# Kernel optimization log

Hardware: AMD Instinct MI355X
Metric: run time of the kernel (lower is better)

The kernel has to match this reference:

```python
import jax, jax.numpy as jnp
import numpy as np

DIM = 256; D_STATE = 16; D_CONV = 4; EXPAND = 2; NS = 64
D_INNER = EXPAND * DIM; DT_RANK = (DIM + 15) // 16
B_SZ = 2; H = 64; W = 64


def setup_inputs() -> dict:
    key = jax.random.key(0)
    ks = jax.random.split(key, 32)
    g = lambda i, shape, s=0.02: jax.random.normal(ks[i], shape, dtype=jnp.float32) * s
    inp = {}
    inp["x"] = jax.random.normal(ks[0], (B_SZ, DIM, H, W), dtype=jnp.float32)
    inp["ln_w"] = jnp.ones((DIM,), jnp.float32)
    inp["ln_b"] = jnp.zeros((DIM,), jnp.float32)
    inp["in_proj_w"] = g(1, (2 * D_INNER, DIM))
    for suf, base in (("", 2), ("_b", 10), ("_s", 18)):
        inp["conv_w" + suf] = g(base, (D_INNER, D_CONV), 0.1)
        inp["conv_b" + suf] = g(base + 1, (D_INNER,), 0.1)
        inp["x_proj_w" + suf] = g(base + 2, (DT_RANK + 2 * D_STATE, D_INNER))
        inp["dt_proj_w" + suf] = g(base + 3, (D_INNER, DT_RANK), 0.1)
        inp["dt_proj_b" + suf] = g(base + 4, (D_INNER,), 0.5)
        inp["D" + suf] = jnp.ones((D_INNER,), jnp.float32)
    A_log = jnp.tile(jnp.log(jnp.arange(1, D_STATE + 1, dtype=jnp.float32)), (D_INNER, 1))
    inp["A_log"] = A_log
    inp["A_log_b"] = A_log
    inp["A_log_s"] = A_log
    inp["out_proj_w"] = g(26, (DIM, D_INNER))
    return inp


def _silu(x):
    return x * jax.nn.sigmoid(x)


def _causal_conv(x, w, b):
    # x: (B, L, D); w: (D, K) depthwise causal conv along L
    K = w.shape[1]; L = x.shape[1]
    xp = jnp.pad(x, ((0, 0), (K - 1, 0), (0, 0)))
    y = b
    for k in range(K):
        y = y + xp[:, k:k + L, :] * w[:, k]
    return y


def _ssm_dir(x, z, conv_w, conv_b, x_proj_w, dt_proj_w, dt_proj_b, A_log, Dp):
    # one directional Mamba inner fn (no out_proj); x, z: (B, L, d_inner)
    Bsz, L, Din = x.shape
    xc = _silu(_causal_conv(x, conv_w, conv_b))
    x_dbl = xc @ x_proj_w.T  # (B, L, dt_rank + 2*d_state)
    dt_r = x_dbl[..., :DT_RANK]
    Bm = x_dbl[..., DT_RANK:DT_RANK + D_STATE]
    Cm = x_dbl[..., DT_RANK + D_STATE:]
    dt = jax.nn.softplus(dt_r @ dt_proj_w.T + dt_proj_b)  # (B, L, d_inner)
    A = -jnp.exp(A_log)  # (d_inner, d_state)

    def step(h, inp):
        dt_t, x_t, B_t, C_t = inp
        dA = jnp.exp(dt_t[..., None] * A)  # (B, d_inner, d_state)
        h = dA * h + (dt_t * x_t)[..., None] * B_t[:, None, :]
        return h, jnp.einsum('bds,bs->bd', h, C_t)

    h0 = jnp.zeros((Bsz, Din, D_STATE), x.dtype)
    _, ys = jax.lax.scan(step, h0, (dt.transpose(1, 0, 2), xc.transpose(1, 0, 2),
                                    Bm.transpose(1, 0, 2), Cm.transpose(1, 0, 2)))
    y = ys.transpose(1, 0, 2) + xc * Dp
    return y * _silu(z)


def reference(x, ln_w, ln_b, in_proj_w,
              conv_w, conv_b, x_proj_w, dt_proj_w, dt_proj_b, D,
              conv_w_b, conv_b_b, x_proj_w_b, dt_proj_w_b, dt_proj_b_b, D_b,
              conv_w_s, conv_b_s, x_proj_w_s, dt_proj_w_s, dt_proj_b_s, D_s,
              A_log, A_log_b, A_log_s, out_proj_w):
    Bsz, C, Hh, Ww = x.shape
    L = Hh * Ww
    xf = x.reshape(Bsz, C, L).transpose(0, 2, 1)  # (B, L, C)
    mu = xf.mean(-1, keepdims=True)
    var = ((xf - mu) ** 2).mean(-1, keepdims=True)
    xn = (xf - mu) / jnp.sqrt(var + 1e-5) * ln_w + ln_b
    xz = xn @ in_proj_w.T  # (B, L, 2*d_inner), shared across directions
    xin, z = xz[..., :D_INNER], xz[..., D_INNER:]
    # forward scan
    y_f = _ssm_dir(xin, z, conv_w, conv_b, x_proj_w, dt_proj_w, dt_proj_b, A_log, D)
    # backward scan (flip sequence, scan, flip back)
    y_b = _ssm_dir(xin[:, ::-1], z[:, ::-1], conv_w_b, conv_b_b, x_proj_w_b,
                   dt_proj_w_b, dt_proj_b_b, A_log_b, D_b)[:, ::-1]
    # slice-interleaved scan: 'b (s i) d -> b (i s) d' with s = NS slices
    def il(t):
        return t.reshape(Bsz, NS, L // NS, D_INNER).transpose(0, 2, 1, 3).reshape(Bsz, L, D_INNER)
    def dil(t):
        return t.reshape(Bsz, L // NS, NS, D_INNER).transpose(0, 2, 1, 3).reshape(Bsz, L, D_INNER)
    y_s = dil(_ssm_dir(il(xin), il(z), conv_w_s, conv_b_s, x_proj_w_s,
                       dt_proj_w_s, dt_proj_b_s, A_log_s, D_s))
    out = (y_f + y_b + y_s) @ out_proj_w.T  # (B, L, C)
    return x + out.transpose(0, 2, 1).reshape(Bsz, C, Hh, Ww)
```

## Files before the change

### kernel.cpp

```cpp
#include <hip/hip_runtime.h>
#include <hip/hip_bf16.h>
#include <cstdint>

#define B_SZ 2
#define DIM 256
#define L_SEQ 4096
#define D_INNER 512
#define DT_RANK 16
#define D_STATE 16
#define NCHUNK 128
#define CHUNK 32

static constexpr size_t SZ_BIG_SH = (size_t)B_SZ * L_SEQ * D_INNER;
static constexpr size_t F_DIR  = (size_t)B_SZ * NCHUNK * D_STATE * D_INNER;
static constexpr size_t SD_DIR = (size_t)B_SZ * NCHUNK * D_INNER;

typedef __attribute__((ext_vector_type(8))) short short8v;
typedef __attribute__((ext_vector_type(4))) short short4v;
typedef __attribute__((ext_vector_type(4))) float f32x4;

__device__ __forceinline__ float silu_f(float v) {
    return v / (1.0f + __expf(-v));
}
__device__ __forceinline__ float softplus_fast(float v) {
    return (v > 15.0f) ? v : __logf(1.0f + __expf(v));
}
__device__ __forceinline__ short f2bf(float f) {
    uint32_t u = __float_as_uint(f);
    u += 0x7fffu + ((u >> 16) & 1u);
    return (short)(u >> 16);
}
__device__ __forceinline__ float bf2f(short s) {
    return __uint_as_float(((uint32_t)(uint16_t)s) << 16);
}
__device__ __forceinline__ int dir_map(int p, int dm) {
    if (dm == 0) return p;
    if (dm == 1) return (L_SEQ - 1) - p;
    return ((p & 63) << 6) | (p >> 6);
}
__device__ __forceinline__ void pow_dA(float r1, float* dA) {
    const float r2 = r1 * r1, r4 = r2 * r2, r8 = r4 * r4;
    dA[0] = r1;         dA[1] = r2;         dA[2] = r2 * r1;    dA[3] = r4;
    dA[4] = r4 * r1;    dA[5] = r4 * r2;    dA[6] = r4 * dA[2]; dA[7] = r8;
    dA[8] = r8 * r1;    dA[9] = r8 * r2;    dA[10] = r8 * dA[2]; dA[11] = r8 * r4;
    dA[12] = r8 * dA[4]; dA[13] = r8 * dA[5]; dA[14] = r8 * dA[6]; dA[15] = r8 * r8;
}

__global__ __launch_bounds__(256) void k_cvt(
    const float* __restrict__ Wi, const float* __restrict__ Wo,
    const float* __restrict__ xp0, const float* __restrict__ xp1, const float* __restrict__ xp2,
    const float* __restrict__ dw0, const float* __restrict__ dw1, const float* __restrict__ dw2,
    short* __restrict__ Wib, short* __restrict__ Wob,
    short* __restrict__ xpwb, short* __restrict__ dtwb)
{
    const int idx = blockIdx.x * 256 + threadIdx.x;
    const float* src; short* dst; int off;
    if (idx < 65536)        { src = Wi; dst = Wib; off = idx; }
    else if (idx < 98304)   { src = Wo; dst = Wob; off = idx - 65536; }
    else if (idx < 116736)  {
        int k = idx - 98304; const int d = k / 6144; k -= d * 6144;
        src = d == 0 ? xp0 : (d == 1 ? xp1 : xp2);
        dst = xpwb + (size_t)d * 24576; off = k;
    } else {
        int k = idx - 116736; const int d = k / 2048; k -= d * 2048;
        src = d == 0 ? dw0 : (d == 1 ? dw1 : dw2);
        dst = dtwb + (size_t)d * 8192; off = k;
    }
    const float4 v = *(const float4*)(src + (size_t)off * 4);
    short4v p = {f2bf(v.x), f2bf(v.y), f2bf(v.z), f2bf(v.w)};
    *(short4v*)(dst + (size_t)off * 4) = p;
}

__global__ __launch_bounds__(256) void k_ln_t(
    const float* __restrict__ x, const float* __restrict__ lnw,
    const float* __restrict__ lnb, short* __restrict__ xnb)
{
    __shared__ float xt[64][257];
    __shared__ float red[2][4][64];
    __shared__ float muS[64], rsS[64];
    __shared__ float lnwS[DIM], lnbS[DIM];

    const int b  = blockIdx.x >> 6;
    const int l0 = (blockIdx.x & 63) << 6;
    const int t  = threadIdx.x;
    lnwS[t] = lnw[t]; lnbS[t] = lnb[t];

    const float* xb = x + (size_t)b * DIM * L_SEQ + l0;
#pragma unroll
    for (int it = 0; it < 16; ++it) {
        const int idx = it * 256 + t;
        const int c = idx >> 4, pos = (idx & 15) << 2;
        const float4 v = *(const float4*)(xb + (size_t)c * L_SEQ + pos);
        xt[pos + 0][c] = v.x; xt[pos + 1][c] = v.y;
        xt[pos + 2][c] = v.z; xt[pos + 3][c] = v.w;
    }
    __syncthreads();
    {
        const int l = t & 63, cq = t >> 6;
        float sum = 0.f, sq = 0.f;
        for (int c = cq * 64; c < cq * 64 + 64; ++c) {
            const float v = xt[l][c];
            sum += v; sq += v * v;
        }
        red[0][cq][l] = sum; red[1][cq][l] = sq;
    }
    __syncthreads();
    if (t < 64) {
        const float s  = red[0][0][t] + red[0][1][t] + red[0][2][t] + red[0][3][t];
        const float q2 = red[1][0][t] + red[1][1][t] + red[1][2][t] + red[1][3][t];
        const float mu  = s * (1.0f / DIM);
        const float var = q2 * (1.0f / DIM) - mu * mu;
        muS[t] = mu; rsS[t] = rsqrtf(var + 1e-5f);
    }
    __syncthreads();
#pragma unroll
    for (int it = 0; it < 32; ++it) {
        const int idx = it * 256 + t;
        const int l = idx >> 7, cp = (idx & 127) << 1;
        const float mu = muS[l], rs = rsS[l];
        short2 p;
        p.x = f2bf((xt[l][cp + 0] - mu) * rs * lnwS[cp + 0] + lnbS[cp + 0]);
        p.y = f2bf((xt[l][cp + 1] - mu) * rs * lnwS[cp + 1] + lnbS[cp + 1]);
        *(short2*)(xnb + (size_t)((b * L_SEQ) + l0 + l) * DIM + cp) = p;
    }
}

__global__ __launch_bounds__(256) void k_inproj_mfma(
    const short* __restrict__ xnb, const short* __restrict__ Wib,
    short* __restrict__ xinb, short* __restrict__ szb)
{
    const int mblk = blockIdx.x >> 2;
    const int q    = blockIdx.x & 3;
    const int t = threadIdx.x;
    const int w = t >> 6, l = t & 63;
    const int m0 = mblk * 64 + w * 16;
    const int n0 = q * 256;
    const int lrow = l & 15, lk = l >> 4;

    short8v a[8];
    {
        const short* ap = xnb + (size_t)(m0 + lrow) * DIM + lk * 8;
#pragma unroll
        for (int kk = 0; kk < 8; ++kk)
            a[kk] = *(const short8v*)(ap + kk * 32);
    }

#pragma unroll 4
    for (int nf = 0; nf < 16; ++nf) {
        const int n = n0 + nf * 16 + lrow;
        const short* bp = Wib + (size_t)n * DIM + lk * 8;
        f32x4 acc = {0.f, 0.f, 0.f, 0.f};
#pragma unroll
        for (int kk = 0; kk < 8; ++kk)
            acc = __builtin_amdgcn_mfma_f32_16x16x32_bf16(
                a[kk], *(const short8v*)(bp + kk * 32), acc, 0, 0, 0);
        const int col = n;
        const int r0  = m0 + lk * 4;
        if (n0 < D_INNER) {
#pragma unroll
            for (int j = 0; j < 4; ++j)
                xinb[(size_t)(r0 + j) * D_INNER + col] = f2bf(acc[j]);
        } else {
#pragma unroll
            for (int j = 0; j < 4; ++j)
                szb[(size_t)(r0 + j) * D_INNER + (col - D_INNER)] = f2bf(silu_f(acc[j]));
        }
    }
}

__global__ __launch_bounds__(256) void k_conv3(
    const short* __restrict__ xinb,
    const float* __restrict__ cw0, const float* __restrict__ cw1, const float* __restrict__ cw2,
    const float* __restrict__ cb0, const float* __restrict__ cb1, const float* __restrict__ cb2,
    short* __restrict__ xcbb, int dir_base, size_t xcb_str)
{
    const int rel = blockIdx.x >> 9;
    const int rem = blockIdx.x & 511;
    const int dir = dir_base + rel;
    const int b   = rem >> 8;
    const int p0  = (rem & 255) << 4;
    const int t   = threadIdx.x;

    const float* cw = dir == 0 ? cw0 : (dir == 1 ? cw1 : cw2);
    const float* cb = dir == 0 ? cb0 : (dir == 1 ? cb1 : cb2);
    short* xcb = xcbb + (size_t)rel * xcb_str;

    __shared__ short s[19][D_INNER];
    for (int i = 0; i < 19; ++i) {
        const int pk = p0 - 3 + i;
        short2 v = {0, 0};
        if (pk >= 0) {
            const int lo = dir_map(pk, dir);
            v = *(const short2*)(xinb + ((size_t)b * L_SEQ + lo) * D_INNER + t * 2);
        }
        *(short2*)&s[i][t * 2] = v;
    }
    __syncthreads();

#pragma unroll
    for (int half = 0; half < 2; ++half) {
        const int d = half * 256 + t;
        const float4 wv = *(const float4*)(cw + d * 4);
        const float bb = cb[d];
        float x0 = bf2f(s[0][d]), x1 = bf2f(s[1][d]), x2 = bf2f(s[2][d]);
#pragma unroll
        for (int i = 0; i < 16; ++i) {
            const float x3 = bf2f(s[i + 3][d]);
            const float a = bb + wv.x * x0 + wv.y * x1 + wv.z * x2 + wv.w * x3;
            xcb[((size_t)b * L_SEQ + p0 + i) * D_INNER + d] = f2bf(silu_f(a));
            x0 = x1; x1 = x2; x2 = x3;
        }
    }
}

__global__ __launch_bounds__(256) void k_proj3_mfma(
    const short* __restrict__ xcbb, const short* __restrict__ xpwb,
    const short* __restrict__ dtwb,
    const float* __restrict__ dtb0, const float* __restrict__ dtb1, const float* __restrict__ dtb2,
    short* __restrict__ dtYb, float* __restrict__ bcbuf,
    int dir_base, size_t xcb_str, size_t bc_str)
{
    const int rel = blockIdx.x >> 9;
    const int rem = blockIdx.x & 511;
    const int dir = dir_base + rel;
    const int m0  = rem * 16;
    const int t = threadIdx.x;
    const int w = t >> 6, l = t & 63;
    const int lrow = l & 15, lk = l >> 4;

    const short* xcb = xcbb + (size_t)rel * xcb_str;
    const short* xpw = xpwb + (size_t)dir * (48 * 512);
    const short* dtw = dtwb + (size_t)dir * (512 * 16);
    const float* dtb = dir == 0 ? dtb0 : (dir == 1 ? dtb1 : dtb2);
    short* dt = dtYb + (size_t)dir * SZ_BIG_SH;
    float* bc = bcbuf + (size_t)rel * bc_str;

    __shared__ float red[4][3][16][17];
    __shared__ short xdblb[16][16];
    __shared__ float dtbS[512];

    dtbS[t] = dtb[t]; dtbS[t + 256] = dtb[t + 256];

    short8v a[4];
    {
        const short* ap = xcb + (size_t)(m0 + lrow) * D_INNER + w * 128 + lk * 8;
#pragma unroll
        for (int kk = 0; kk < 4; ++kk)
            a[kk] = *(const short8v*)(ap + kk * 32);
    }

#pragma unroll
    for (int nf = 0; nf < 3; ++nf) {
        f32x4 acc = {0.f, 0.f, 0.f, 0.f};
        const short* bp = xpw + (size_t)(nf * 16 + lrow) * D_INNER + w * 128 + lk * 8;
#pragma unroll
        for (int kk = 0; kk < 4; ++kk)
            acc = __builtin_amdgcn_mfma_f32_16x16x32_bf16(
                a[kk], *(const short8v*)(bp + kk * 32), acc, 0, 0, 0);
#pragma unroll
        for (int j = 0; j < 4; ++j)
            red[w][nf][lk * 4 + j][lrow] = acc[j];
    }
    __syncthreads();

#pragma unroll
    for (int i = 0; i < 3; ++i) {
        const int nf = i;
        const int row = (t >> 4) & 15, col = t & 15;
        const float v = red[0][nf][row][col] + red[1][nf][row][col]
                      + red[2][nf][row][col] + red[3][nf][row][col];
        if (nf == 0) xdblb[row][col] = f2bf(v);
        else         bc[(size_t)(m0 + row) * 32 + (nf - 1) * 16 + col] = v;
    }
    __syncthreads();

    short8v adt = {0, 0, 0, 0, 0, 0, 0, 0};
    if (lk < 2) adt = *(const short8v*)&xdblb[lrow][lk * 8];

#pragma unroll
    for (int nbw = 0; nbw < 8; ++nbw) {
        const int nb = w * 8 + nbw;
        short8v bdt = {0, 0, 0, 0, 0, 0, 0, 0};
        if (lk < 2) bdt = *(const short8v*)(dtw + (size_t)(nb * 16 + lrow) * 16 + lk * 8);
        f32x4 acc = {0.f, 0.f, 0.f, 0.f};
        acc = __builtin_amdgcn_mfma_f32_16x16x32_bf16(adt, bdt, acc, 0, 0, 0);
        const int d = nb * 16 + lrow;
        const float bias = dtbS[d];
#pragma unroll
        for (int j = 0; j < 4; ++j)
            dt[(size_t)(m0 + lk * 4 + j) * D_INNER + d] = f2bf(softplus_fast(acc[j] + bias));
    }
}

__device__ __forceinline__ bool fast_vote(const float* Al_d, int t, int* flagS) {
    bool ok = true;
    const float a0 = __expf(Al_d[0]);
#pragma unroll
    for (int s = 1; s < 16; ++s) {
        const float v = __expf(Al_d[s]);
        const float e = (float)(s + 1) * a0;
        ok = ok && (fabsf(v - e) <= 1e-3f * e);
    }
    if (t == 0) *flagS = 1;
    __syncthreads();
    if (!ok) *flagS = 0;
    __syncthreads();
    return *flagS != 0;
}

template<bool FAST>
__device__ __forceinline__ void scan1_body(
    const short* dtp, const short* xcp, const float* bcp,
    short (*dts)[256], short (*xcs)[256], float (*bcs)[16],
    const float* Al_d, int t, short* F_o, float* SD_o)
{
    float As20, As2[16];
    if (FAST) {
        As20 = -__expf(Al_d[0]) * 1.44269504f;
    } else {
#pragma unroll
        for (int s = 0; s < 16; ++s) As2[s] = -__expf(Al_d[s]) * 1.44269504f;
        As20 = As2[0];
    }
    float h[16];
#pragma unroll
    for (int s = 0; s < 16; ++s) h[s] = 0.f;
    float sumdt = 0.f;

    for (int tile = 0; tile < CHUNK / 16; ++tile) {
        const int p0 = tile * 16;
#pragma unroll
        for (int rep = 0; rep < 2; ++rep) {
            const int idx = rep * 256 + t;
            const int jr = idx >> 5, c8 = (idx & 31) << 3;
            *(short8v*)&dts[jr][c8] = *(const short8v*)(dtp + (size_t)(p0 + jr) * D_INNER + c8);
            *(short8v*)&xcs[jr][c8] = *(const short8v*)(xcp + (size_t)(p0 + jr) * D_INNER + c8);
        }
        if (t < 64) {
            const int jr = t >> 2, c4 = (t & 3) << 2;
            *(float4*)&bcs[jr][c4] = *(const float4*)(bcp + (size_t)(p0 + jr) * 32 + c4);
        }
        __syncthreads();

#pragma unroll
        for (int j = 0; j < 16; ++j) {
            const float dtv = bf2f(dts[j][t]);
            const float xv  = bf2f(xcs[j][t]);
            sumdt += dtv;
            const float dtx = dtv * xv;
            float Bv[16];
#pragma unroll
            for (int s4 = 0; s4 < 4; ++s4) {
                const float4 bb = *(const float4*)&bcs[j][s4 * 4];
                Bv[s4 * 4 + 0] = bb.x; Bv[s4 * 4 + 1] = bb.y;
                Bv[s4 * 4 + 2] = bb.z; Bv[s4 * 4 + 3] = bb.w;
            }
            if (FAST) {
                float dA[16];
                pow_dA(exp2f(dtv * As20), dA);
#pragma unroll
                for (int s = 0; s < 16; ++s)
                    h[s] = fmaf(dA[s], h[s], dtx * Bv[s]);
            } else {
#pragma unroll
                for (int s = 0; s < 16; ++s)
                    h[s] = fmaf(exp2f(dtv * As2[s]), h[s], dtx * Bv[s]);
            }
        }
        __syncthreads();
    }
#pragma unroll
    for (int s = 0; s < 16; ++s)
        F_o[(size_t)s * D_INNER] = f2bf(h[s]);
    *SD_o = sumdt;
}

template<bool FAST>
__device__ __forceinline__ void scan2_body(
    short* dtp, const short* xcp, const float* bcp,
    short (*dts)[256], short (*xcs)[256], float (*bcs)[32],
    const float* Al_d, int t, float Dv, const short* Hin_o)
{
    float As20, As2[16];
    if (FAST) {
        As20 = -__expf(Al_d[0]) * 1.44269504f;
    } else {
#pragma unroll
        for (int s = 0; s < 16; ++s) As2[s] = -__expf(Al_d[s]) * 1.44269504f;
        As20 = As2[0];
    }
    float h[16];
#pragma unroll
    for (int s = 0; s < 16; ++s)
        h[s] = bf2f(Hin_o[(size_t)s * D_INNER]);

    for (int tile = 0; tile < CHUNK / 16; ++tile) {
        const int p0 = tile * 16;
#pragma unroll
        for (int rep = 0; rep < 2; ++rep) {
            const int idx = rep * 256 + t;
            const int jr = idx >> 5, c8 = (idx & 31) << 3;
            *(short8v*)&dts[jr][c8] = __builtin_nontemporal_load(
                (const short8v*)(dtp + (size_t)(p0 + jr) * D_INNER + c8));
            *(short8v*)&xcs[jr][c8] = __builtin_nontemporal_load(
                (const short8v*)(xcp + (size_t)(p0 + jr) * D_INNER + c8));
        }
        if (t < 128) {
            const int jr = t >> 3, c4 = (t & 7) << 2;
            *(float4*)&bcs[jr][c4] = *(const float4*)(bcp + (size_t)(p0 + jr) * 32 + c4);
        }
        __syncthreads();

#pragma unroll
        for (int j = 0; j < 16; ++j) {
            const float dtv = bf2f(dts[j][t]);
            const float xv  = bf2f(xcs[j][t]);
            const float dtx = dtv * xv;
            float Bv[16], Cv[16];
#pragma unroll
            for (int s4 = 0; s4 < 4; ++s4) {
                const float4 bb = *(const float4*)&bcs[j][s4 * 4];
                const float4 cc = *(const float4*)&bcs[j][16 + s4 * 4];
                Bv[s4 * 4 + 0] = bb.x; Bv[s4 * 4 + 1] = bb.y;
                Bv[s4 * 4 + 2] = bb.z; Bv[s4 * 4 + 3] = bb.w;
                Cv[s4 * 4 + 0] = cc.x; Cv[s4 * 4 + 1] = cc.y;
                Cv[s4 * 4 + 2] = cc.z; Cv[s4 * 4 + 3] = cc.w;
            }
            float y = xv * Dv;
            if (FAST) {
                float dA[16];
                pow_dA(exp2f(dtv * As20), dA);
#pragma unroll
                for (int s = 0; s < 16; ++s) {
                    h[s] = fmaf(dA[s], h[s], dtx * Bv[s]);
                    y = fmaf(h[s], Cv[s], y);
                }
            } else {
#pragma unroll
                for (int s = 0; s < 16; ++s) {
                    h[s] = fmaf(exp2f(dtv * As2[s]), h[s], dtx * Bv[s]);
                    y = fmaf(h[s], Cv[s], y);
                }
            }
            __builtin_nontemporal_store(f2bf(y), dtp + (size_t)(p0 + j) * D_INNER + t);
        }
        __syncthreads();
    }
}

__global__ __launch_bounds__(256, 4) void k_scan1(
    const short* __restrict__ dtYb, const short* __restrict__ xcbb,
    const float* __restrict__ bcb,
    const float* __restrict__ Al0, const float* __restrict__ Al1, const float* __restrict__ Al2,
    short* __restrict__ Fg, float* __restrict__ SDg,
    int dir_base, size_t xcb_str, size_t bc_str)
{
    const int rel = blockIdx.x >> 9;
    const int rem = blockIdx.x & 511;
    const int dir = dir_base + rel;
    const int b     = rem >> 8;
    const int chunk = (rem >> 1) & 127;
    const int half  = rem & 1;
    const int t = threadIdx.x;
    const int d = half * 256 + t;

    const short* dtg = dtYb + (size_t)dir * SZ_BIG_SH;
    const short* xcg = xcbb + (size_t)rel * xcb_str;
    const float* bcg = bcb + (size_t)rel * bc_str;
    const float* Al = dir == 0 ? Al0 : (dir == 1 ? Al1 : Al2);
    short* F  = Fg  + (size_t)rel * F_DIR;
    float* SD = SDg + (size_t)rel * SD_DIR;

    __shared__ short dts[16][256];
    __shared__ short xcs[16][256];
    __shared__ float bcs[16][16];
    __shared__ int flagS;

    const size_t rowbase = (size_t)b * L_SEQ + chunk * CHUNK;
    const short* dtp = dtg + rowbase * D_INNER + half * 256;
    const short* xcp = xcg + rowbase * D_INNER + half * 256;
    const float* bcp = bcg + rowbase * 32;
    const float* Al_d = Al + d * D_STATE;
    const size_t fo  = ((size_t)b * NCHUNK + chunk) * (D_STATE * D_INNER) + d;
    const size_t sdo = ((size_t)b * NCHUNK + chunk) * D_INNER + d;

    const bool fast = fast_vote(Al_d, t, &flagS);
    if (fast) scan1_body<true >(dtp, xcp, bcp, dts, xcs, bcs, Al_d, t, F + fo, SD + sdo);
    else      scan1_body<false>(dtp, xcp, bcp, dts, xcs, bcs, Al_d, t, F + fo, SD + sdo);
}

__global__ __launch_bounds__(256) void k_comb(
    short* __restrict__ Fg, const float* __restrict__ SDg,
    const float* __restrict__ Al0, const float* __restrict__ Al1, const float* __restrict__ Al2,
    int dir_base)
{
    const int rel = blockIdx.x >> 6;
    const int dir = dir_base + rel;
    const int gid = (blockIdx.x & 63) * 256 + threadIdx.x;
    const int b   = gid >> 13;
    const int rem = gid & 8191;
    const int s   = rem >> 9;
    const int d   = rem & 511;

    const float* Al = dir == 0 ? Al0 : (dir == 1 ? Al1 : Al2);
    const float As2 = -__expf(Al[d * D_STATE + s]) * 1.44269504f;

    short* F        = Fg  + (size_t)rel * F_DIR;
    const float* SD = SDg + (size_t)rel * SD_DIR;

    float h = 0.f;
    for (int c = 0; c < NCHUNK; ++c) {
        const size_t base = (size_t)(b * NCHUNK + c);
        const size_t i  = (base << 13) + rem;
        const float sd  = SD[(base << 9) + d];
        const float P   = exp2f(As2 * sd);
        const float fv  = bf2f(F[i]);
        F[i] = f2bf(h);
        h = fmaf(P, h, fv);
    }
}

__global__ __launch_bounds__(256, 4) void k_scan2(
    short* dtYb,
    const short* __restrict__ xcbb, const float* __restrict__ bcb,
    const float* __restrict__ Al0, const float* __restrict__ Al1, const float* __restrict__ Al2,
    const float* __restrict__ Dp0, const float* __restrict__ Dp1, const float* __restrict__ Dp2,
    const short* __restrict__ Hing,
    int dir_base, size_t xcb_str, size_t bc_str)
{
    const int rel = blockIdx.x >> 9;
    const int rem = blockIdx.x & 511;
    const int dir = dir_base + rel;
    const int b     = rem >> 8;
    const int chunk = (rem >> 1) & 127;
    const int half  = rem & 1;
    const int t = threadIdx.x;
    const int d = half * 256 + t;

    short* dtg      = dtYb + (size_t)dir * SZ_BIG_SH;
    const short* xcg = xcbb + (size_t)rel * xcb_str;
    const float* bcg = bcb + (size_t)rel * bc_str;
    const float* Al  = dir == 0 ? Al0 : (dir == 1 ? Al1 : Al2);
    const float* Dpp = dir == 0 ? Dp0 : (dir == 1 ? Dp1 : Dp2);
    const short* Hin = Hing + (size_t)rel * F_DIR;

    __shared__ short dts[16][256];
    __shared__ short xcs[16][256];
    __shared__ float bcs[16][32];
    __shared__ int flagS;

    const size_t rowbase = (size_t)b * L_SEQ + chunk * CHUNK;
    short* dtp       = dtg + rowbase * D_INNER + half * 256;
    const short* xcp = xcg + rowbase * D_INNER + half * 256;
    const float* bcp = bcg + rowbase * 32;
    const float* Al_d = Al + d * D_STATE;
    const float Dv = Dpp[d];
    const size_t fo = ((size_t)b * NCHUNK + chunk) * (D_STATE * D_INNER) + d;

    const bool fast = fast_vote(Al_d, t, &flagS);
    if (fast) scan2_body<true >(dtp, xcp, bcp, dts, xcs, bcs, Al_d, t, Dv, Hin + fo);
    else      scan2_body<false>(dtp, xcp, bcp, dts, xcs, bcs, Al_d, t, Dv, Hin + fo);
}

__global__ __launch_bounds__(256) void k_out3_mfma(
    const short* __restrict__ yall, const short* __restrict__ szb,
    const short* __restrict__ Wob, const float* __restrict__ x,
    float* __restrict__ out)
{
    __shared__ short ytb[32][512];
    const int tile = blockIdx.x;
    const int b  = tile >> 7;
    const int l0 = (tile & 127) << 5;
    const int t  = threadIdx.x;

    const short* y0 = yall;
    const short* y1 = yall + SZ_BIG_SH;
    const short* y2 = yall + 2 * SZ_BIG_SH;
    const size_t rb = (size_t)b * L_SEQ;

#pragma unroll
    for (int it = 0; it < 8; ++it) {
        const int idx = it * 256 + t;
        const int r  = idx >> 6;
        const int c8 = idx & 63;
        const int lrow = l0 + r;
        const int p1 = (L_SEQ - 1) - lrow;
        const int p2 = ((lrow & 63) << 6) | (lrow >> 6);
        const short8v s0 = *(const short8v*)(y0 + (rb + lrow) * D_INNER + c8 * 8);
        const short8v s1 = *(const short8v*)(y1 + (rb + p1)   * D_INNER + c8 * 8);
        const short8v s2 = *(const short8v*)(y2 + (rb + p2)   * D_INNER + c8 * 8);
        const short8v sv = *(const short8v*)(szb + (rb + lrow) * D_INNER + c8 * 8);
        short8v pk;
#pragma unroll
        for (int i = 0; i < 8; ++i)
            pk[i] = f2bf((bf2f(s0[i]) + bf2f(s1[i]) + bf2f(s2[i])) * bf2f(sv[i]));
        *(short8v*)&ytb[r][(c8 ^ (r & 7)) * 8] = pk;
    }
    __syncthreads();

    const int w = t >> 6, l = t & 63;
    const int lrow = l & 15, lk = l >> 4;
    const int nf = w & 1;
    const int j0 = (w >> 1) * 128;
    const int brow = nf * 16 + lrow;

    f32x4 acc[8];
#pragma unroll
    for (int jf = 0; jf < 8; ++jf) acc[jf] = {0.f, 0.f, 0.f, 0.f};

#pragma unroll 4
    for (int kk = 0; kk < 16; ++kk) {
        const int c8 = kk * 4 + lk;
        const short8v bfrag = *(const short8v*)&ytb[brow][(c8 ^ (brow & 7)) * 8];
#pragma unroll
        for (int jf = 0; jf < 8; ++jf) {
            const short8v afrag = *(const short8v*)(
                Wob + (size_t)(j0 + jf * 16 + lrow) * D_INNER + kk * 32 + lk * 8);
            acc[jf] = __builtin_amdgcn_mfma_f32_16x16x32_bf16(afrag, bfrag, acc[jf], 0, 0, 0);
        }
    }

    const int lcol = l0 + nf * 16 + lrow;
#pragma unroll
    for (int jf = 0; jf < 8; ++jf) {
        const int jr0 = j0 + jf * 16 + lk * 4;
#pragma unroll
        for (int j = 0; j < 4; ++j) {
            const size_t o = ((size_t)b * DIM + jr0 + j) * L_SEQ + lcol;
            out[o] = x[o] + acc[jf][j];
        }
    }
}

extern "C" void kernel_launch(void* const* d_in, const int* in_sizes, int n_in,
                              void* d_out, int out_size, void* d_ws, size_t ws_size,
                              hipStream_t stream)
{
    const float* x       = (const float*)d_in[0];
    const float* ln_w    = (const float*)d_in[1];
    const float* ln_b    = (const float*)d_in[2];
    const float* in_proj = (const float*)d_in[3];
    const float* conv_w[3] = {(const float*)d_in[4],  (const float*)d_in[10], (const float*)d_in[16]};
    const float* conv_b[3] = {(const float*)d_in[5],  (const float*)d_in[11], (const float*)d_in[17]};
    const float* xpw[3]    = {(const float*)d_in[6],  (const float*)d_in[12], (const float*)d_in[18]};
    const float* dtw[3]    = {(const float*)d_in[7],  (const float*)d_in[13], (const float*)d_in[19]};
    const float* dtb[3]    = {(const float*)d_in[8],  (const float*)d_in[14], (const float*)d_in[20]};
    const float* Dp[3]     = {(const float*)d_in[9],  (const float*)d_in[15], (const float*)d_in[21]};
    const float* A_log[3]  = {(const float*)d_in[22], (const float*)d_in[23], (const float*)d_in[24]};
    const float* out_proj  = (const float*)d_in[25];
    float* out = (float*)d_out;
    (void)in_sizes; (void)n_in; (void)out_size;

    const size_t NROW   = (size_t)B_SZ * L_SEQ;
    const size_t SZ_XNB = NROW * DIM / 2;
    const size_t SZ_WIB = 262144 / 2;
    const size_t SZ_WOB = 131072 / 2;
    const size_t SZ_XPW = 3 * 24576 / 2;
    const size_t SZ_DTW = 3 * 8192 / 2;
    const size_t SZ_BH  = NROW * D_INNER / 2;
    const size_t SZ_BC  = NROW * 32;
    const size_t SZ_F   = F_DIR / 2;

    const size_t need_merged =
        SZ_XNB + SZ_WIB + SZ_WOB + SZ_XPW + SZ_DTW +
        2 * SZ_BH + 3 * SZ_BH + 3 * SZ_BH + 3 * SZ_BC +
        3 * (SZ_F + SD_DIR);
    const bool merged = ws_size >= need_merged * sizeof(float);
    const int ndir = merged ? 3 : 1;
    const size_t xcb_str = merged ? (SZ_BH * 2) : 0;
    const size_t bc_str  = merged ? SZ_BC : 0;

    float* ws   = (float*)d_ws;
    float* p    = ws;
    short* xnb  = (short*)p;  p += SZ_XNB;
    short* Wib  = (short*)p;  p += SZ_WIB;
    short* Wob  = (short*)p;  p += SZ_WOB;
    short* xpwb = (short*)p;  p += SZ_XPW;
    short* dtwb = (short*)p;  p += SZ_DTW;
    short* xinb = (short*)p;  p += SZ_BH;
    short* szb  = (short*)p;  p += SZ_BH;
    short* dtYb = (short*)p;  p += 3 * SZ_BH;
    short* xcbb = (short*)p;  p += (size_t)ndir * SZ_BH;
    float* bc   = p;          p += (size_t)ndir * SZ_BC;
    short* Fg   = (short*)p;  p += (size_t)ndir * SZ_F;
    float* SDg  = p;          p += (size_t)ndir * SD_DIR;

    k_cvt<<<dim3(480), dim3(256), 0, stream>>>(
        in_proj, out_proj, xpw[0], xpw[1], xpw[2], dtw[0], dtw[1], dtw[2],
        Wib, Wob, xpwb, dtwb);
    k_ln_t<<<dim3(B_SZ * 64), dim3(256), 0, stream>>>(x, ln_w, ln_b, xnb);
    k_inproj_mfma<<<dim3(512), dim3(256), 0, stream>>>(xnb, Wib, xinb, szb);

    for (int d0 = 0; d0 < 3; d0 += ndir) {
        k_conv3<<<dim3(512 * ndir), dim3(256), 0, stream>>>(
            xinb, conv_w[0], conv_w[1], conv_w[2],
            conv_b[0], conv_b[1], conv_b[2], xcbb, d0, xcb_str);
        k_proj3_mfma<<<dim3(512 * ndir), dim3(256), 0, stream>>>(
            xcbb, xpwb, dtwb, dtb[0], dtb[1], dtb[2],
            dtYb, bc, d0, xcb_str, bc_str);
        k_scan1<<<dim3(512 * ndir), dim3(256), 0, stream>>>(
            dtYb, xcbb, bc, A_log[0], A_log[1], A_log[2], Fg, SDg,
            d0, xcb_str, bc_str);
        k_comb<<<dim3(64 * ndir), dim3(256), 0, stream>>>(
            Fg, SDg, A_log[0], A_log[1], A_log[2], d0);
        k_scan2<<<dim3(512 * ndir), dim3(256), 0, stream>>>(
            dtYb, xcbb, bc, A_log[0], A_log[1], A_log[2],
            Dp[0], Dp[1], Dp[2], Fg, d0, xcb_str, bc_str);
    }

    k_out3_mfma<<<dim3(256), dim3(256), 0, stream>>>(
        dtYb, szb, Wob, x, out);
}
```

Measured before the change: 232.8 us.

## Fuse x/dt projection with chunk-local scan pass and halve chunk length

Merges the projection kernel with the first chunked-scan pass. The dt, xc and B/C tiles for a 16-row chunk stay in shared memory (dt with an XOR swizzle) and feed the local scan directly, so the scan no longer re-reads them from global memory and one launch per direction goes away. The chunk size drops from 32 to 16, which doubles the chunk count. That doubles the work of the serial chunk-combine pass and the size of the F/SD buffers, and each fused block now has every thread scan two channels, adding shared memory and register pressure.

Result: slower. 261.6 us (+12.4%).

```diff
diff --git a/kernel.cpp b/kernel.cpp
--- a/kernel.cpp
+++ b/kernel.cpp
@@ -8,8 +8,8 @@
 #define D_INNER 512
 #define DT_RANK 16
 #define D_STATE 16
-#define NCHUNK 128
-#define CHUNK 32
+#define NCHUNK 256
+#define CHUNK 16
 
 static constexpr size_t SZ_BIG_SH = (size_t)B_SZ * L_SEQ * D_INNER;
 static constexpr size_t F_DIR  = (size_t)B_SZ * NCHUNK * D_STATE * D_INNER;
@@ -213,17 +213,70 @@
     }
 }
 
-__global__ __launch_bounds__(256) void k_proj3_mfma(
+template<bool FAST>
+__device__ __forceinline__ void chunk_scan_local(
+    const short (*dtS)[512], const short (*xcS)[512], const float (*bcsS)[32],
+    const float* Al_d, int d, short* F_o, float* SD_o)
+{
+    float As20, As2[16];
+    if (FAST) {
+        As20 = -__expf(Al_d[0]) * 1.44269504f;
+    } else {
+#pragma unroll
+        for (int s = 0; s < 16; ++s) As2[s] = -__expf(Al_d[s]) * 1.44269504f;
+        As20 = As2[0];
+    }
+    float h[16];
+#pragma unroll
+    for (int s = 0; s < 16; ++s) h[s] = 0.f;
+    float sumdt = 0.f;
+
+#pragma unroll
+    for (int j = 0; j < 16; ++j) {
+        const float dtv = bf2f(dtS[j][d ^ (j << 3)]);
+        const float xv  = bf2f(xcS[j][d]);
+        sumdt += dtv;
+        const float dtx = dtv * xv;
+        float Bv[16];
+#pragma unroll
+        for (int s4 = 0; s4 < 4; ++s4) {
+            const float4 bb = *(const float4*)&bcsS[j][s4 * 4];
+            Bv[s4 * 4 + 0] = bb.x; Bv[s4 * 4 + 1] = bb.y;
+            Bv[s4 * 4 + 2] = bb.z; Bv[s4 * 4 + 3] = bb.w;
+        }
+        if (FAST) {
+            float dA[16];
+            pow_dA(exp2f(dtv * As20), dA);
+#pragma unroll
+            for (int s = 0; s < 16; ++s)
+                h[s] = fmaf(dA[s], h[s], dtx * Bv[s]);
+        } else {
+#pragma unroll
+            for (int s = 0; s < 16; ++s)
+                h[s] = fmaf(exp2f(dtv * As2[s]), h[s], dtx * Bv[s]);
+        }
+    }
+#pragma unroll
+    for (int s = 0; s < 16; ++s)
+        F_o[(size_t)s * D_INNER] = f2bf(h[s]);
+    *SD_o = sumdt;
+}
+
+__global__ __launch_bounds__(256) void k_proj_scan1(
     const short* __restrict__ xcbb, const short* __restrict__ xpwb,
     const short* __restrict__ dtwb,
     const float* __restrict__ dtb0, const float* __restrict__ dtb1, const float* __restrict__ dtb2,
+    const float* __restrict__ Al0, const float* __restrict__ Al1, const float* __restrict__ Al2,
     short* __restrict__ dtYb, float* __restrict__ bcbuf,
+    short* __restrict__ Fg, float* __restrict__ SDg,
     int dir_base, size_t xcb_str, size_t bc_str)
 {
     const int rel = blockIdx.x >> 9;
     const int rem = blockIdx.x & 511;
     const int dir = dir_base + rel;
     const int m0  = rem * 16;
+    const int b     = rem >> 8;
+    const int chunk = rem & 255;
     const int t = threadIdx.x;
     const int w = t >> 6, l = t & 63;
     const int lrow = l & 15, lk = l >> 4;
@@ -232,14 +285,29 @@
     const short* xpw = xpwb + (size_t)dir * (48 * 512);
     const short* dtw = dtwb + (size_t)dir * (512 * 16);
     const float* dtb = dir == 0 ? dtb0 : (dir == 1 ? dtb1 : dtb2);
+    const float* Al  = dir == 0 ? Al0 : (dir == 1 ? Al1 : Al2);
     short* dt = dtYb + (size_t)dir * SZ_BIG_SH;
     float* bc = bcbuf + (size_t)rel * bc_str;
-
+    short* F  = Fg  + (size_t)rel * F_DIR;
+    float* SD = SDg + (size_t)rel * SD_DIR;
+
+    __shared__ short xcS[16][512];
+    __shared__ short dtS[16][512];
     __shared__ float red[4][3][16][17];
     __shared__ short xdblb[16][16];
+    __shared__ float bcsS[16][32];
     __shared__ float dtbS[512];
-
+    __shared__ int flagS;
+
+#pragma unroll
+    for (int it = 0; it < 4; ++it) {
+        const int idx = it * 256 + t;
+        const int jr = idx >> 6, c8 = idx & 63;
+        *(short8v*)&xcS[jr][c8 * 8] =
+            *(const short8v*)(xcb + (size_t)(m0 + jr) * D_INNER + c8 * 8);
+    }
     dtbS[t] = dtb[t]; dtbS[t + 256] = dtb[t + 256];
+    __syncthreads();
 
     short8v a[4];
     {
@@ -269,8 +337,12 @@
         const int row = (t >> 4) & 15, col = t & 15;
         const float v = red[0][nf][row][col] + red[1][nf][row][col]
                       + red[2][nf][row][col] + red[3][nf][row][col];
-        if (nf == 0) xdblb[row][col] = f2bf(v);
-        else         bc[(size_t)(m0 + row) * 32 + (nf - 1) * 16 + col] = v;
+        if (nf == 0) {
+            xdblb[row][col] = f2bf(v);
+        } else {
+            bc[(size_t)(m0 + row) * 32 + (nf - 1) * 16 + col] = v;
+            bcsS[row][(nf - 1) * 16 + col] = v;
+        }
     }
     __syncthreads();
 
@@ -284,209 +356,50 @@
         if (lk < 2) bdt = *(const short8v*)(dtw + (size_t)(nb * 16 + lrow) * 16 + lk * 8);
         f32x4 acc = {0.f, 0.f, 0.f, 0.f};
         acc = __builtin_amdgcn_mfma_f32_16x16x32_bf16(adt, bdt, acc, 0, 0, 0);
-        const int d = nb * 16 + lrow;
-        const float bias = dtbS[d];
-#pragma unroll
-        for (int j = 0; j < 4; ++j)
-            dt[(size_t)(m0 + lk * 4 + j) * D_INNER + d] = f2bf(softplus_fast(acc[j] + bias));
-    }
-}
-
-__device__ __forceinline__ bool fast_vote(const float* Al_d, int t, int* flagS) {
+        const int dd = nb * 16 + lrow;
+        const float bias = dtbS[dd];
+#pragma unroll
+        for (int j = 0; j < 4; ++j) {
+            const int row = lk * 4 + j;
+            const short v = f2bf(softplus_fast(acc[j] + bias));
+            dt[(size_t)(m0 + row) * D_INNER + dd] = v;
+            dtS[row][dd ^ (row << 3)] = v;
+        }
+    }
+    __syncthreads();
+
     bool ok = true;
-    const float a0 = __expf(Al_d[0]);
-#pragma unroll
-    for (int s = 1; s < 16; ++s) {
-        const float v = __expf(Al_d[s]);
-        const float e = (float)(s + 1) * a0;
-        ok = ok && (fabsf(v - e) <= 1e-3f * e);
-    }
-    if (t == 0) *flagS = 1;
-    __syncthreads();
-    if (!ok) *flagS = 0;
-    __syncthreads();
-    return *flagS != 0;
-}
-
-template<bool FAST>
-__device__ __forceinline__ void scan1_body(
-    const short* dtp, const short* xcp, const float* bcp,
-    short (*dts)[256], short (*xcs)[256], float (*bcs)[16],
-    const float* Al_d, int t, short* F_o, float* SD_o)
-{
-    float As20, As2[16];
-    if (FAST) {
-        As20 = -__expf(Al_d[0]) * 1.44269504f;
+    {
+        const float* a0p = Al + t * D_STATE;
+        const float* a1p = Al + (t + 256) * D_STATE;
+        const float e00 = __expf(a0p[0]), e10 = __expf(a1p[0]);
+#pragma unroll
+        for (int s = 1; s < 16; ++s) {
+            const float v0 = __expf(a0p[s]), ex0 = (float)(s + 1) * e00;
+            const float v1 = __expf(a1p[s]), ex1 = (float)(s + 1) * e10;
+            ok = ok && (fabsf(v0 - ex0) <= 1e-3f * ex0)
+                    && (fabsf(v1 - ex1) <= 1e-3f * ex1);
+        }
+    }
+    if (t == 0) flagS = 1;
+    __syncthreads();
+    if (!ok) flagS = 0;
+    __syncthreads();
+    const bool fast = flagS != 0;
+
+    const size_t fbase  = ((size_t)b * NCHUNK + chunk) * (D_STATE * D_INNER);
+    const size_t sdbase = ((size_t)b * NCHUNK + chunk) * D_INNER;
+    if (fast) {
+        chunk_scan_local<true >(dtS, xcS, bcsS, Al + t * D_STATE, t,
+                                F + fbase + t, SD + sdbase + t);
+        chunk_scan_local<true >(dtS, xcS, bcsS, Al + (t + 256) * D_STATE, t + 256,
+                                F + fbase + t + 256, SD + sdbase + t + 256);
     } else {
-#pragma unroll
-        for (int s = 0; s < 16; ++s) As2[s] = -__expf(Al_d[s]) * 1.44269504f;
-        As20 = As2[0];
-    }
-    float h[16];
-#pragma unroll
-    for (int s = 0; s < 16; ++s) h[s] = 0.f;
-    float sumdt = 0.f;
-
-    for (int tile = 0; tile < CHUNK / 16; ++tile) {
-        const int p0 = tile * 16;
-#pragma unroll
-        for (int rep = 0; rep < 2; ++rep) {
-            const int idx = rep * 256 + t;
-            const int jr = idx >> 5, c8 = (idx & 31) << 3;
-            *(short8v*)&dts[jr][c8] = *(const short8v*)(dtp + (size_t)(p0 + jr) * D_INNER + c8);
-            *(short8v*)&xcs[jr][c8] = *(const short8v*)(xcp + (size_t)(p0 + jr) * D_INNER + c8);
-        }
-        if (t < 64) {
-            const int jr = t >> 2, c4 = (t & 3) << 2;
-            *(float4*)&bcs[jr][c4] = *(const float4*)(bcp + (size_t)(p0 + jr) * 32 + c4);
-        }
-        __syncthreads();
-
-#pragma unroll
-        for (int j = 0; j < 16; ++j) {
-            const float dtv = bf2f(dts[j][t]);
-            const float xv  = bf2f(xcs[j][t]);
-            sumdt += dtv;
-            const float dtx = dtv * xv;
-            float Bv[16];
-#pragma unroll
-            for (int s4 = 0; s4 < 4; ++s4) {
-                const float4 bb = *(const float4*)&bcs[j][s4 * 4];
-                Bv[s4 * 4 + 0] = bb.x; Bv[s4 * 4 + 1] = bb.y;
-                Bv[s4 * 4 + 2] = bb.z; Bv[s4 * 4 + 3] = bb.w;
-            }
-            if (FAST) {
-                float dA[16];
-                pow_dA(exp2f(dtv * As20), dA);
-#pragma unroll
-                for (int s = 0; s < 16; ++s)
-                    h[s] = fmaf(dA[s], h[s], dtx * Bv[s]);
-            } else {
-#pragma unroll
-                for (int s = 0; s < 16; ++s)
-                    h[s] = fmaf(exp2f(dtv * As2[s]), h[s], dtx * Bv[s]);
-            }
-        }
-        __syncthreads();
-    }
-#pragma unroll
-    for (int s = 0; s < 16; ++s)
-        F_o[(size_t)s * D_INNER] = f2bf(h[s]);
-    *SD_o = sumdt;
-}
-
-template<bool FAST>
-__device__ __forceinline__ void scan2_body(
-    short* dtp, const short* xcp, const float* bcp,
-    short (*dts)[256], short (*xcs)[256], float (*bcs)[32],
-    const float* Al_d, int t, float Dv, const short* Hin_o)
-{
-    float As20, As2[16];
-    if (FAST) {
-        As20 = -__expf(Al_d[0]) * 1.44269504f;
-    } else {
-#pragma unroll
-        for (int s = 0; s < 16; ++s) As2[s] = -__expf(Al_d[s]) * 1.44269504f;
-        As20 = As2[0];
-    }
-    float h[16];
-#pragma unroll
-    for (int s = 0; s < 16; ++s)
-        h[s] = bf2f(Hin_o[(size_t)s * D_INNER]);
-
-    for (int tile = 0; tile < CHUNK / 16; ++tile) {
-        const int p0 = tile * 16;
-#pragma unroll
-        for (int rep = 0; rep < 2; ++rep) {
-            const int idx = rep * 256 + t;
-            const int jr = idx >> 5, c8 = (idx & 31) << 3;
-            *(short8v*)&dts[jr][c8] = __builtin_nontemporal_load(
-                (const short8v*)(dtp + (size_t)(p0 + jr) * D_INNER + c8));
-            *(short8v*)&xcs[jr][c8] = __builtin_nontemporal_load(
-                (const short8v*)(xcp + (size_t)(p0 + jr) * D_INNER + c8));
-        }
-        if (t < 128) {
-            const int jr = t >> 3, c4 = (t & 7) << 2;
-            *(float4*)&bcs[jr][c4] = *(const float4*)(bcp + (size_t)(p0 + jr) * 32 + c4);
-        }
-        __syncthreads();
-
-#pragma unroll
-        for (int j = 0; j < 16; ++j) {
-            const float dtv = bf2f(dts[j][t]);
-            const float xv  = bf2f(xcs[j][t]);
-            const float dtx = dtv * xv;
-            float Bv[16], Cv[16];
-#pragma unroll
-            for (int s4 = 0; s4 < 4; ++s4) {
-                const float4 bb = *(const float4*)&bcs[j][s4 * 4];
-                const float4 cc = *(const float4*)&bcs[j][16 + s4 * 4];
-                Bv[s4 * 4 + 0] = bb.x; Bv[s4 * 4 + 1] = bb.y;
-                Bv[s4 * 4 + 2] = bb.z; Bv[s4 * 4 + 3] = bb.w;
-                Cv[s4 * 4 + 0] = cc.x; Cv[s4 * 4 + 1] = cc.y;
-                Cv[s4 * 4 + 2] = cc.z; Cv[s4 * 4 + 3] = cc.w;
-            }
-            float y = xv * Dv;
-            if (FAST) {
-                float dA[16];
-                pow_dA(exp2f(dtv * As20), dA);
-#pragma unroll
-                for (int s = 0; s < 16; ++s) {
-                    h[s] = fmaf(dA[s], h[s], dtx * Bv[s]);
-                    y = fmaf(h[s], Cv[s], y);
-                }
-            } else {
-#pragma unroll
-                for (int s = 0; s < 16; ++s) {
-                    h[s] = fmaf(exp2f(dtv * As2[s]), h[s], dtx * Bv[s]);
-                    y = fmaf(h[s], Cv[s], y);
-                }
-            }
-            __builtin_nontemporal_store(f2bf(y), dtp + (size_t)(p0 + j) * D_INNER + t);
-        }
-        __syncthreads();
-    }
-}
-
-__global__ __launch_bounds__(256, 4) void k_scan1(
-    const short* __restrict__ dtYb, const short* __restrict__ xcbb,
-    const float* __restrict__ bcb,
-    const float* __restrict__ Al0, const float* __restrict__ Al1, const float* __restrict__ Al2,
-    short* __restrict__ Fg, float* __restrict__ SDg,
-    int dir_base, size_t xcb_str, size_t bc_str)
-{
-    const int rel = blockIdx.x >> 9;
-    const int rem = blockIdx.x & 511;
-    const int dir = dir_base + rel;
-    const int b     = rem >> 8;
-    const int chunk = (rem >> 1) & 127;
-    const int half  = rem & 1;
-    const int t = threadIdx.x;
-    const int d = half * 256 + t;
-
-    const short* dtg = dtYb + (size_t)dir * SZ_BIG_SH;
-    const short* xcg = xcbb + (size_t)rel * xcb_str;
-    const float* bcg = bcb + (size_t)rel * bc_str;
-    const float* Al = dir == 0 ? Al0 : (dir == 1 ? Al1 : Al2);
-    short* F  = Fg  + (size_t)rel * F_DIR;
-    float* SD = SDg + (size_t)rel * SD_DIR;
-
-    __shared__ short dts[16][256];
-    __shared__ short xcs[16][256];
-    __shared__ float bcs[16][16];
-    __shared__ int flagS;
-
-    const size_t rowbase = (size_t)b * L_SEQ + chunk * CHUNK;
-    const short* dtp = dtg + rowbase * D_INNER + half * 256;
-    const short* xcp = xcg + rowbase * D_INNER + half * 256;
-    const float* bcp = bcg + rowbase * 32;
-    const float* Al_d = Al + d * D_STATE;
-    const size_t fo  = ((size_t)b * NCHUNK + chunk) * (D_STATE * D_INNER) + d;
-    const size_t sdo = ((size_t)b * NCHUNK + chunk) * D_INNER + d;
-
-    const bool fast = fast_vote(Al_d, t, &flagS);
-    if (fast) scan1_body<true >(dtp, xcp, bcp, dts, xcs, bcs, Al_d, t, F + fo, SD + sdo);
-    else      scan1_body<false>(dtp, xcp, bcp, dts, xcs, bcs, Al_d, t, F + fo, SD + sdo);
+        chunk_scan_local<false>(dtS, xcS, bcsS, Al + t * D_STATE, t,
+                                F + fbase + t, SD + sdbase + t);
+        chunk_scan_local<false>(dtS, xcS, bcsS, Al + (t + 256) * D_STATE, t + 256,
+                                F + fbase + t + 256, SD + sdbase + t + 256);
+    }
 }
 
 __global__ __launch_bounds__(256) void k_comb(
@@ -520,6 +433,92 @@
     }
 }
 
+template<bool FAST>
+__device__ __forceinline__ void scan2_body(
+    short* dtp, const short* xcp, const float* bcp,
+    short (*dts)[256], short (*xcs)[256], float (*bcs)[32],
+    const float* Al_d, int t, float Dv, const short* Hin_o)
+{
+    float As20, As2[16];
+    if (FAST) {
+        As20 = -__expf(Al_d[0]) * 1.44269504f;
+    } else {
+#pragma unroll
+        for (int s = 0; s < 16; ++s) As2[s] = -__expf(Al_d[s]) * 1.44269504f;
+        As20 = As2[0];
+    }
+    float h[16];
+#pragma unroll
+    for (int s = 0; s < 16; ++s)
+        h[s] = bf2f(Hin_o[(size_t)s * D_INNER]);
+
+#pragma unroll
+    for (int rep = 0; rep < 2; ++rep) {
+        const int idx = rep * 256 + t;
+        const int jr = idx >> 5, c8 = (idx & 31) << 3;
+        *(short8v*)&dts[jr][c8] = __builtin_nontemporal_load(
+            (const short8v*)(dtp + (size_t)jr * D_INNER + c8));
+        *(short8v*)&xcs[jr][c8] = __builtin_nontemporal_load(
+            (const short8v*)(xcp + (size_t)jr * D_INNER + c8));
+    }
+    if (t < 128) {
+        const int jr = t >> 3, c4 = (t & 7) << 2;
+        *(float4*)&bcs[jr][c4] = *(const float4*)(bcp + (size_t)jr * 32 + c4);
+    }
+    __syncthreads();
+
+#pragma unroll
+    for (int j = 0; j < 16; ++j) {
+        const float dtv = bf2f(dts[j][t]);
+        const float xv  = bf2f(xcs[j][t]);
+        const float dtx = dtv * xv;
+        float Bv[16], Cv[16];
+#pragma unroll
+        for (int s4 = 0; s4 < 4; ++s4) {
+            const float4 bb = *(const float4*)&bcs[j][s4 * 4];
+            const float4 cc = *(const float4*)&bcs[j][16 + s4 * 4];
+            Bv[s4 * 4 + 0] = bb.x; Bv[s4 * 4 + 1] = bb.y;
+            Bv[s4 * 4 + 2] = bb.z; Bv[s4 * 4 + 3] = bb.w;
+            Cv[s4 * 4 + 0] = cc.x; Cv[s4 * 4 + 1] = cc.y;
+            Cv[s4 * 4 + 2] = cc.z; Cv[s4 * 4 + 3] = cc.w;
+        }
+        float y = xv * Dv;
+        if (FAST) {
+            float dA[16];
+            pow_dA(exp2f(dtv * As20), dA);
+#pragma unroll
+            for (int s = 0; s < 16; ++s) {
+                h[s] = fmaf(dA[s], h[s], dtx * Bv[s]);
+                y = fmaf(h[s], Cv[s], y);
+            }
+        } else {
+#pragma unroll
+            for (int s = 0; s < 16; ++s) {
+                h[s] = fmaf(exp2f(dtv * As2[s]), h[s], dtx * Bv[s]);
+                y = fmaf(h[s], Cv[s], y);
+            }
+        }
+        __builtin_nontemporal_store(f2bf(y), dtp + (size_t)j * D_INNER + t);
+    }
+    __syncthreads();
+}
+
+__device__ __forceinline__ bool fast_vote(const float* Al_d, int t, int* flagS) {
+    bool ok = true;
+    const float a0 = __expf(Al_d[0]);
+#pragma unroll
+    for (int s = 1; s < 16; ++s) {
+        const float v = __expf(Al_d[s]);
+        const float e = (float)(s + 1) * a0;
+        ok = ok && (fabsf(v - e) <= 1e-3f * e);
+    }
+    if (t == 0) *flagS = 1;
+    __syncthreads();
+    if (!ok) *flagS = 0;
+    __syncthreads();
+    return *flagS != 0;
+}
+
 __global__ __launch_bounds__(256, 4) void k_scan2(
     short* dtYb,
     const short* __restrict__ xcbb, const float* __restrict__ bcb,
@@ -528,11 +527,11 @@
     const short* __restrict__ Hing,
     int dir_base, size_t xcb_str, size_t bc_str)
 {
-    const int rel = blockIdx.x >> 9;
-    const int rem = blockIdx.x & 511;
+    const int rel = blockIdx.x >> 10;
+    const int rem = blockIdx.x & 1023;
     const int dir = dir_base + rel;
-    const int b     = rem >> 8;
-    const int chunk = (rem >> 1) & 127;
+    const int b     = rem >> 9;
+    const int chunk = (rem >> 1) & 255;
     const int half  = rem & 1;
     const int t = threadIdx.x;
     const int d = half * 256 + t;
@@ -695,15 +694,13 @@
         k_conv3<<<dim3(512 * ndir), dim3(256), 0, stream>>>(
             xinb, conv_w[0], conv_w[1], conv_w[2],
             conv_b[0], conv_b[1], conv_b[2], xcbb, d0, xcb_str);
-        k_proj3_mfma<<<dim3(512 * ndir), dim3(256), 0, stream>>>(
+        k_proj_scan1<<<dim3(512 * ndir), dim3(256), 0, stream>>>(
             xcbb, xpwb, dtwb, dtb[0], dtb[1], dtb[2],
-            dtYb, bc, d0, xcb_str, bc_str);
-        k_scan1<<<dim3(512 * ndir), dim3(256), 0, stream>>>(
-            dtYb, xcbb, bc, A_log[0], A_log[1], A_log[2], Fg, SDg,
-            d0, xcb_str, bc_str);
+            A_log[0], A_log[1], A_log[2],
+            dtYb, bc, Fg, SDg, d0, xcb_str, bc_str);
         k_comb<<<dim3(64 * ndir), dim3(256), 0, stream>>>(
             Fg, SDg, A_log[0], A_log[1], A_log[2], d0);
-        k_scan2<<<dim3(512 * ndir), dim3(256), 0, stream>>>(
+        k_scan2<<<dim3(1024 * ndir), dim3(256), 0, stream>>>(
             dtYb, xcbb, bc, A_log[0], A_log[1], A_log[2],
             Dp[0], Dp[1], Dp[2], Fg, d0, xcb_str, bc_str);
     }
```
